# Optimization experiments

Measured on AMD Instinct MI355X. Metric: run time of the kernel, lower is better.

Reference implementation:

```python
import jax, jax.numpy as jnp
import numpy as np

N_HEADS = 8
HIDDEN = 256
D_HEAD = HIDDEN // N_HEADS
N_NODES = 4096
N_EDGES = 16384


def setup_inputs() -> dict:
    key = jax.random.key(0)
    ks = jax.random.split(key, 12)
    s = 0.05
    return {
        "q": jax.random.normal(ks[0], (N_EDGES, HIDDEN), jnp.float32),
        "k": jax.random.normal(ks[1], (N_NODES, HIDDEN), jnp.float32),
        "v": jax.random.normal(ks[2], (N_NODES, HIDDEN), jnp.float32),
        "T": jax.random.uniform(ks[3], (N_NODES, N_EDGES), jnp.float32),
        "Wq": jax.random.normal(ks[4], (HIDDEN, HIDDEN), jnp.float32) * s,
        "bq": jax.random.normal(ks[5], (HIDDEN,), jnp.float32) * s,
        "Wk": jax.random.normal(ks[6], (HIDDEN, HIDDEN), jnp.float32) * s,
        "bk": jax.random.normal(ks[7], (HIDDEN,), jnp.float32) * s,
        "Wv": jax.random.normal(ks[8], (HIDDEN, HIDDEN), jnp.float32) * s,
        "bv": jax.random.normal(ks[9], (HIDDEN,), jnp.float32) * s,
        "Wo": jax.random.normal(ks[10], (HIDDEN, HIDDEN), jnp.float32) * s,
        "bo": jax.random.normal(ks[11], (HIDDEN,), jnp.float32) * s,
    }


def reference(q, k, v, T, Wq, bq, Wk, bk, Wv, bv, Wo, bo):
    scale = D_HEAD ** (-0.5)
    # projections, reshaped to per-head layout
    qh = (q @ Wq.T + bq).reshape(-1, N_HEADS, D_HEAD)  # [E, H, d]
    kh = (k @ Wk.T + bk).reshape(-1, N_HEADS, D_HEAD)  # [N, H, d]
    vh = (v @ Wv.T + bv).reshape(-1, N_HEADS, D_HEAD)  # [N, H, d]
    # row-normalized transition matrix (rows with zero sum left unscaled)
    row_sum = jnp.sum(T, axis=-1, keepdims=True)       # [N, 1]
    Tn = T / jnp.where(row_sum == 0, 1.0, row_sum)     # [N, E]
    # edge->node aggregation of queries, then scale
    qn = jnp.einsum("ne,ehd->nhd", Tn, qh) * scale     # [N, H, d]
    # attention: full NxN scores per head
    scores = jnp.einsum("nhd,mhd->hnm", qn, kh)        # [H, N, N]
    attn = jax.nn.softmax(scores, axis=-1)
    ctx = jnp.einsum("hnm,mhd->nhd", attn, vh)         # [N, H, d]
    out = ctx.reshape(-1, N_HEADS * D_HEAD) @ Wo.T + bo  # [N, hidden]
    return out
```

## Files before the change

kernel.cpp:

```cpp
#include <hip/hip_runtime.h>


#define N_NODES 4096
#define N_EDGES 16384
#define HIDDEN  256
#define KSPLIT  16

typedef __attribute__((ext_vector_type(4))) float f32x4;
typedef __attribute__((ext_vector_type(8))) short s16x8;
typedef __attribute__((ext_vector_type(4))) unsigned short u16x4;
typedef __attribute__((ext_vector_type(8))) unsigned short u16x8;

__device__ __forceinline__ unsigned short f2bf(float f) {
    union { float f; unsigned u; } x; x.f = f;
    unsigned r = x.u + 0x7FFFu + ((x.u >> 16) & 1u);
    return (unsigned short)(r >> 16);
}
__device__ __forceinline__ s16x8 pack8s(f32x4 x, f32x4 y) {
    u16x8 o;
    o[0]=f2bf(x[0]); o[1]=f2bf(x[1]); o[2]=f2bf(x[2]); o[3]=f2bf(x[3]);
    o[4]=f2bf(y[0]); o[5]=f2bf(y[1]); o[6]=f2bf(y[2]); o[7]=f2bf(y[3]);
    union { u16x8 u; s16x8 s; } c; c.u = o; return c.s;
}

template<int MODE>
__global__ __launch_bounds__(256)
void proj_gemm(const float* __restrict__ A, const float* __restrict__ W,
               const float* __restrict__ bias, void* __restrict__ outp, int M)
{
    __shared__ __align__(16) float As[16][68];
    __shared__ __align__(16) float Ws[16][68];
    const int t  = threadIdx.x;
    const int bm = blockIdx.x * 64, bn = blockIdx.y * 64;
    const int tm = t & 15, tn = t >> 4;
    const int sm = t >> 2, skc = (t & 3) * 4;

    float c[4][4] = {};
    for (int k0 = 0; k0 < 256; k0 += 16) {
        f32x4 av = *(const f32x4*)&A[(long)(bm + sm) * 256 + k0 + skc];
        f32x4 wv = *(const f32x4*)&W[(bn + sm) * 256 + k0 + skc];
        __syncthreads();
        #pragma unroll
        for (int i = 0; i < 4; ++i) { As[skc + i][sm] = av[i]; Ws[skc + i][sm] = wv[i]; }
        __syncthreads();
        #pragma unroll
        for (int kk = 0; kk < 16; ++kk) {
            f32x4 a4 = *(const f32x4*)&As[kk][tm * 4];
            f32x4 w4 = *(const f32x4*)&Ws[kk][tn * 4];
            #pragma unroll
            for (int i = 0; i < 4; ++i)
                #pragma unroll
                for (int j = 0; j < 4; ++j)
                    c[i][j] = fmaf(a4[i], w4[j], c[i][j]);
        }
    }
    f32x4 b4 = *(const f32x4*)&bias[bn + tn * 4];
    if (MODE == 1) {
        unsigned short* out = (unsigned short*)outp;
        #pragma unroll
        for (int i = 0; i < 4; ++i) {
            u16x4 o;
            #pragma unroll
            for (int j = 0; j < 4; ++j) o[j] = f2bf(c[i][j] + b4[j]);
            *(u16x4*)&out[(long)(bm + tm * 4 + i) * 256 + bn + tn * 4] = o;
        }
    } else {
        unsigned short* out = (unsigned short*)outp;
        #pragma unroll
        for (int j = 0; j < 4; ++j) {
            u16x4 o;
            #pragma unroll
            for (int i = 0; i < 4; ++i) o[i] = f2bf(c[i][j] + b4[j]);
            *(u16x4*)&out[(long)(bn + tn * 4 + j) * M + bm + tm * 4] = o;
        }
    }
}

__global__ __launch_bounds__(256)
void proj_out_merge(const float* __restrict__ pctx, const float* __restrict__ plp,
                    const float* __restrict__ W, const float* __restrict__ bias,
                    float* __restrict__ out)
{
    __shared__ __align__(16) float As[16][68];
    __shared__ __align__(16) float Ws[16][68];
    const int t  = threadIdx.x;
    const int bm = blockIdx.x * 64, bn = blockIdx.y * 64;
    const int tm = t & 15, tn = t >> 4;
    const int sm = t >> 2, skc = (t & 3) * 4;
    const int row = bm + sm;

    float c[4][4] = {};
    for (int k0 = 0; k0 < 256; k0 += 16) {
        const int kk0 = k0 + skc, h = kk0 >> 5;
        f32x4 c0 = *(const f32x4*)&pctx[(long)row * 256 + kk0];
        f32x4 c1 = *(const f32x4*)&pctx[(long)(N_NODES + row) * 256 + kk0];
        float lsum = plp[h * N_NODES + row] + plp[(8 + h) * N_NODES + row];
        f32x4 av = (c0 + c1) * (1.0f / lsum);
        f32x4 wv = *(const f32x4*)&W[(bn + sm) * 256 + k0 + skc];
        __syncthreads();
        #pragma unroll
        for (int i = 0; i < 4; ++i) { As[skc + i][sm] = av[i]; Ws[skc + i][sm] = wv[i]; }
        __syncthreads();
        #pragma unroll
        for (int kk = 0; kk < 16; ++kk) {
            f32x4 a4 = *(const f32x4*)&As[kk][tm * 4];
            f32x4 w4 = *(const f32x4*)&Ws[kk][tn * 4];
            #pragma unroll
            for (int i = 0; i < 4; ++i)
                #pragma unroll
                for (int j = 0; j < 4; ++j)
                    c[i][j] = fmaf(a4[i], w4[j], c[i][j]);
        }
    }
    f32x4 b4 = *(const f32x4*)&bias[bn + tn * 4];
    #pragma unroll
    for (int i = 0; i < 4; ++i) {
        f32x4 o;
        #pragma unroll
        for (int j = 0; j < 4; ++j) o[j] = c[i][j] + b4[j];
        *(f32x4*)&out[(long)(bm + tm * 4 + i) * 256 + bn + tn * 4] = o;
    }
}

__global__ __launch_bounds__(512)
void proj_q_mfma(const float* __restrict__ A, const float* __restrict__ W,
                 const float* __restrict__ bias, unsigned short* __restrict__ outT)
{
    __shared__ __align__(16) unsigned short Wsm[256 * 264];
    __shared__ __align__(16) unsigned short Asm[64 * 72];
    const int t  = threadIdx.x;
    const int m0 = blockIdx.x * 64;

    const int am = t >> 3, akc = (t & 7) * 8;
    const float* Arow = &A[(long)(m0 + am) * 256];
    f32x4 a0 = *(const f32x4*)&Arow[akc];
    f32x4 a1 = *(const f32x4*)&Arow[akc + 4];

    #pragma unroll 4
    for (int i = 0; i < 32; ++i) {
        const int g = i * 512 + t;
        const int row = g >> 6, col = (g & 63) * 4;
        f32x4 w4 = *(const f32x4*)&W[row * 256 + col];
        u16x4 o;
        #pragma unroll
        for (int j = 0; j < 4; ++j) o[j] = f2bf(w4[j]);
        *(u16x4*)&Wsm[row * 264 + col] = o;
    }

    const int l = t & 63, lo = l & 15, h4 = l >> 4;
    const int wv = t >> 6, wm = (wv >> 2) * 32, wn = (wv & 3) * 64;
    f32x4 acc[2][4] = {};

    for (int k0 = 0; k0 < 4; ++k0) {
        u16x4 p0, p1;
        #pragma unroll
        for (int j = 0; j < 4; ++j) { p0[j] = f2bf(a0[j]); p1[j] = f2bf(a1[j]); }
        *(u16x4*)&Asm[am * 72 + akc]     = p0;
        *(u16x4*)&Asm[am * 72 + akc + 4] = p1;
        __syncthreads();
        if (k0 < 3) {
            a0 = *(const f32x4*)&Arow[(k0 + 1) * 64 + akc];
            a1 = *(const f32x4*)&Arow[(k0 + 1) * 64 + akc + 4];
        }
        s16x8 af[2][2], wf[4][2];
        #pragma unroll
        for (int mi = 0; mi < 2; ++mi)
            #pragma unroll
            for (int k2 = 0; k2 < 2; ++k2)
                af[mi][k2] = *(const s16x8*)&Asm[(wm + mi * 16 + lo) * 72 + k2 * 32 + h4 * 8];
        #pragma unroll
        for (int nj = 0; nj < 4; ++nj)
            #pragma unroll
            for (int k2 = 0; k2 < 2; ++k2)
                wf[nj][k2] = *(const s16x8*)&Wsm[(wn + nj * 16 + lo) * 264 + k0 * 64 + k2 * 32 + h4 * 8];
        #pragma unroll
        for (int k2 = 0; k2 < 2; ++k2)
            #pragma unroll
            for (int mi = 0; mi < 2; ++mi)
                #pragma unroll
                for (int nj = 0; nj < 4; ++nj)
                    acc[mi][nj] = __builtin_amdgcn_mfma_f32_16x16x32_bf16(
                        af[mi][k2], wf[nj][k2], acc[mi][nj], 0, 0, 0);
        __syncthreads();
    }
    float bi[4];
    #pragma unroll
    for (int nj = 0; nj < 4; ++nj) bi[nj] = bias[wn + nj * 16 + lo];
    #pragma unroll
    for (int mi = 0; mi < 2; ++mi)
        #pragma unroll
        for (int nj = 0; nj < 4; ++nj) {
            u16x4 o;
            #pragma unroll
            for (int r = 0; r < 4; ++r) o[r] = f2bf(acc[mi][nj][r] + bi[nj]);
            const int  n = wn + nj * 16 + lo;
            const long m = m0 + wm + mi * 16 + h4 * 4;
            *(u16x4*)&outT[(long)n * N_EDGES + m] = o;
        }
}

__global__ __launch_bounds__(512, 4)
void tgemm(const float* __restrict__ T, const unsigned short* __restrict__ Bt,
           float* __restrict__ part, float* __restrict__ rsp)
{
    __shared__ __align__(16) unsigned short Bsm[2][256 * 64];
    const int t  = threadIdx.x;
    const int ks = blockIdx.x & 15, ms = blockIdx.x >> 4;
    const int m0 = ms * 128;
    const long k00 = (long)ks * 1024;
    const int w = t >> 6, l = t & 63, lo = l & 15, h4 = l >> 4;

    const int kx = ((l & 7) * 8) ^ ((l >> 3) << 3);
    const unsigned short* Bsrc = Bt + k00 + kx;

#define STAGE(itv, bufv) do {                                                       \
    const unsigned short* _s = Bsrc + (long)(itv) * 64;                             \
    unsigned short* _d = &Bsm[(bufv)][w * 2048];                                    \
    _Pragma("unroll")                                                               \
    for (int _i = 0; _i < 4; ++_i)                                                  \
        __builtin_amdgcn_global_load_lds(                                           \
            (const __attribute__((address_space(1))) unsigned int*)                 \
                (_s + (long)(w * 32 + _i * 8 + (l >> 3)) * N_EDGES),                \
            (__attribute__((address_space(3))) unsigned int*)(_d + _i * 512),       \
            16, 0, 0);                                                              \
} while (0)

    const float* Arow = T + (long)(m0 + w * 16 + lo) * N_EDGES + k00 + h4 * 8;

    STAGE(0, 0);
    f32x4 a0 = *(const f32x4*)&Arow[0];
    f32x4 a1 = *(const f32x4*)&Arow[4];
    f32x4 a2 = *(const f32x4*)&Arow[32];
    f32x4 a3 = *(const f32x4*)&Arow[36];
    __syncthreads();

    f32x4 acc[16] = {};
    float rs = 0.f;

    for (int it = 0; it < 16; ++it) {
        const int cur = it & 1;
        if (it < 15) STAGE(it + 1, cur ^ 1);
        s16x8 af0 = pack8s(a0, a1);
        s16x8 af1 = pack8s(a2, a3);
        rs += a0[0]+a0[1]+a0[2]+a0[3] + a1[0]+a1[1]+a1[2]+a1[3]
            + a2[0]+a2[1]+a2[2]+a2[3] + a3[0]+a3[1]+a3[2]+a3[3];
        if (it < 15) {
            const float* An = Arow + (it + 1) * 64;
            a0 = *(const f32x4*)&An[0];
            a1 = *(const f32x4*)&An[4];
            a2 = *(const f32x4*)&An[32];
            a3 = *(const f32x4*)&An[36];
        }
        const unsigned short* Bb = Bsm[cur];
        const int swz = (lo & 7) << 3;
        #pragma unroll
        for (int nj = 0; nj < 16; ++nj) {
            const int jb = (nj * 16 + lo) * 64;
            s16x8 bf0 = *(const s16x8*)&Bb[jb + ((h4 * 8) ^ swz)];
            s16x8 bf1 = *(const s16x8*)&Bb[jb + ((32 + h4 * 8) ^ swz)];
            acc[nj] = __builtin_amdgcn_mfma_f32_16x16x32_bf16(af0, bf0, acc[nj], 0, 0, 0);
            acc[nj] = __builtin_amdgcn_mfma_f32_16x16x32_bf16(af1, bf1, acc[nj], 0, 0, 0);
        }
        __syncthreads();
    }
#undef STAGE

    rs += __shfl_xor(rs, 16); rs += __shfl_xor(rs, 32);
    if (h4 == 0) rsp[ks * N_NODES + m0 + w * 16 + lo] = rs;

    float* P = part + (long)ks * (N_NODES * HIDDEN);
    #pragma unroll
    for (int nj = 0; nj < 16; ++nj)
        #pragma unroll
        for (int r = 0; r < 4; ++r)
            P[(long)(m0 + w * 16 + h4 * 4 + r) * HIDDEN + nj * 16 + lo] = acc[nj][r];
}

__global__ __launch_bounds__(256)
void finalize(const float* __restrict__ part, const float* __restrict__ rsp,
              unsigned short* __restrict__ qn)
{
    const int idx = blockIdx.x * 256 + threadIdx.x;
    const long i4 = (long)idx * 4;
    const int n = (int)(i4 >> 8);
    f32x4 s = {};
    #pragma unroll
    for (int ksp = 0; ksp < KSPLIT; ++ksp)
        s += *(const f32x4*)&part[(long)ksp * (N_NODES * HIDDEN) + i4];
    float rs = 0.f;
    #pragma unroll
    for (int ksp = 0; ksp < KSPLIT; ++ksp) rs += rsp[ksp * N_NODES + n];
    rs = (rs == 0.0f) ? 1.0f : rs;
    const float sc = 0.17677669529663687f / rs;
    u16x4 o;
    #pragma unroll
    for (int i = 0; i < 4; ++i) o[i] = f2bf(s[i] * sc);
    *(u16x4*)&qn[i4] = o;
}

__global__ __launch_bounds__(256)
void attn(const unsigned short* __restrict__ qn, const unsigned short* __restrict__ kh,
          const unsigned short* __restrict__ vht, float* __restrict__ pctx,
          float* __restrict__ plp)
{
    __shared__ __align__(16) unsigned short Ksm[64 * 40];
    __shared__ __align__(16) unsigned short Vsm[32 * 72];
    __shared__ __align__(16) unsigned short Psm[4][32 * 72];
    const int t  = threadIdx.x;
    const int hh = blockIdx.x >> 6, nb = (blockIdx.x >> 1) & 31, mh = blockIdx.x & 1;
    const int w = t >> 6, l = t & 63, lo = l & 15, h4 = l >> 4;
    const int n0 = nb * 128 + w * 32;

    const int km = t >> 2, kdc = (t & 3) * 8;
    const int vd = t >> 3, vmc = (t & 7) * 8;

    s16x8 qf[2];
    #pragma unroll
    for (int ni = 0; ni < 2; ++ni)
        qf[ni] = *(const s16x8*)&qn[(long)(n0 + ni * 16 + lo) * HIDDEN + hh * 32 + h4 * 8];

    f32x4 acc[2][2] = {};
    float lp[2][4] = {};
    const f32x4 zero = {};

    for (int mt = mh * 32; mt < mh * 32 + 32; ++mt) {
        const int m0 = mt * 64;
        *(s16x8*)&Ksm[km * 40 + kdc] =
            *(const s16x8*)&kh[(long)(m0 + km) * HIDDEN + hh * 32 + kdc];
        *(s16x8*)&Vsm[vd * 72 + vmc] =
            *(const s16x8*)&vht[(long)(hh * 32 + vd) * N_NODES + m0 + vmc];
        __syncthreads();

        s16x8 kb[4];
        #pragma unroll
        for (int mi = 0; mi < 4; ++mi)
            kb[mi] = *(const s16x8*)&Ksm[(mi * 16 + lo) * 40 + h4 * 8];
        #pragma unroll
        for (int ni = 0; ni < 2; ++ni) {
            #pragma unroll
            for (int mi = 0; mi < 4; ++mi) {
                f32x4 s = __builtin_amdgcn_mfma_f32_16x16x32_bf16(qf[ni], kb[mi], zero, 0, 0, 0);
                #pragma unroll
                for (int r = 0; r < 4; ++r) {
                    float p = __expf(s[r]);
                    lp[ni][r] += p;
                    Psm[w][(ni * 16 + h4 * 4 + r) * 72 + mi * 16 + lo] = f2bf(p);
                }
            }
        }
        s16x8 pa[2][2], vb[2][2];
        #pragma unroll
        for (int ni = 0; ni < 2; ++ni)
            #pragma unroll
            for (int k2 = 0; k2 < 2; ++k2)
                pa[ni][k2] = *(const s16x8*)&Psm[w][(ni * 16 + lo) * 72 + k2 * 32 + h4 * 8];
        #pragma unroll
        for (int di = 0; di < 2; ++di)
            #pragma unroll
            for (int k2 = 0; k2 < 2; ++k2)
                vb[di][k2] = *(const s16x8*)&Vsm[(di * 16 + lo) * 72 + k2 * 32 + h4 * 8];
        #pragma unroll
        for (int k2 = 0; k2 < 2; ++k2)
            #pragma unroll
            for (int ni = 0; ni < 2; ++ni)
                #pragma unroll
                for (int di = 0; di < 2; ++di)
                    acc[ni][di] = __builtin_amdgcn_mfma_f32_16x16x32_bf16(
                        pa[ni][k2], vb[di][k2], acc[ni][di], 0, 0, 0);
        __syncthreads();
    }
    #pragma unroll
    for (int ni = 0; ni < 2; ++ni)
        #pragma unroll
        for (int r = 0; r < 4; ++r) {
            float v2 = lp[ni][r];
            v2 += __shfl_xor(v2, 1); v2 += __shfl_xor(v2, 2);
            v2 += __shfl_xor(v2, 4); v2 += __shfl_xor(v2, 8);
            lp[ni][r] = v2;
        }
    float* myctx = pctx + (long)mh * (N_NODES * HIDDEN);
    float* myplp = plp  + (long)(mh * 8 + hh) * N_NODES;
    if (lo == 0)
        #pragma unroll
        for (int ni = 0; ni < 2; ++ni)
            #pragma unroll
            for (int r = 0; r < 4; ++r)
                myplp[n0 + ni * 16 + h4 * 4 + r] = lp[ni][r];
    #pragma unroll
    for (int ni = 0; ni < 2; ++ni)
        #pragma unroll
        for (int di = 0; di < 2; ++di)
            #pragma unroll
            for (int r = 0; r < 4; ++r)
                myctx[(long)(n0 + ni * 16 + h4 * 4 + r) * HIDDEN + hh * 32 + di * 16 + lo]
                    = acc[ni][di][r];
}

extern "C" void kernel_launch(void* const* d_in, const int* in_sizes, int n_in,
                              void* d_out, int out_size, void* d_ws, size_t ws_size,
                              hipStream_t stream)
{
    const float* q  = (const float*)d_in[0];
    const float* k  = (const float*)d_in[1];
    const float* v  = (const float*)d_in[2];
    const float* T  = (const float*)d_in[3];
    const float* Wq = (const float*)d_in[4];  const float* bq = (const float*)d_in[5];
    const float* Wk = (const float*)d_in[6];  const float* bk = (const float*)d_in[7];
    const float* Wv = (const float*)d_in[8];  const float* bv = (const float*)d_in[9];
    const float* Wo = (const float*)d_in[10]; const float* bo = (const float*)d_in[11];

    char* w = (char*)d_ws;
    unsigned short* qh_t = (unsigned short*)(w);
    unsigned short* kh   = (unsigned short*)(w + (8u  << 20));
    unsigned short* vh_t = (unsigned short*)(w + (10u << 20));
    unsigned short* qn   = (unsigned short*)(w + (12u << 20));
    float*          pctx = (float*)         (w + (14u << 20));
    float*          plp  = (float*)         (w + (22u << 20));
    float*          part = (float*)         (w + (24u << 20));
    float*          rsp  = (float*)         (w + (88u << 20));

    proj_q_mfma<<<256, 512, 0, stream>>>(q, Wq, bq, qh_t);
    proj_gemm<1><<<dim3(64, 4),  256, 0, stream>>>(k, Wk, bk, kh,   N_NODES);
    proj_gemm<2><<<dim3(64, 4),  256, 0, stream>>>(v, Wv, bv, vh_t, N_NODES);
    tgemm<<<512, 512, 0, stream>>>(T, qh_t, part, rsp);
    finalize<<<1024, 256, 0, stream>>>(part, rsp, qn);
    attn<<<512, 256, 0, stream>>>(qn, kh, vh_t, pctx, plp);
    proj_out_merge<<<dim3(64, 4), 256, 0, stream>>>(pctx, plp, Wo, bo, (float*)d_out);
}
```

Measured before the change: 230.8 us.

## Move projections to bf16 MFMA and split attention keys four ways

Adds a kernel that converts all four weight matrices to bf16 once, then replaces the fp32 FMA GEMMs for the K, V and output projections, and the LDS-staged Q projection, with register-only MFMA kernels that read A directly from global memory. The attention grid doubles to 1024 blocks, each covering a quarter of the key range, and the output projection now merges four partial contexts and softmax denominators. The aim is to raise matrix-core use and occupancy in the projections and attention. In exchange it adds a kernel launch, more partial-sum memory traffic, and fp32 inputs rounded to bf16 in the K, V and output projections.

```diff
diff --git a/kernel.cpp b/kernel.cpp
--- a/kernel.cpp
+++ b/kernel.cpp
@@ -23,180 +23,105 @@
     union { u16x8 u; s16x8 s; } c; c.u = o; return c.s;
 }
 
+__global__ __launch_bounds__(256)
+void cvtW(const float* __restrict__ Wq, const float* __restrict__ Wk,
+          const float* __restrict__ Wv, const float* __restrict__ Wo,
+          unsigned short* __restrict__ dst)
+{
+    const int g = blockIdx.x * 256 + threadIdx.x;
+    const long base = (long)g * 8;
+    const int mat = (int)(base >> 16), off = (int)(base & 65535);
+    const float* src = (mat == 0) ? Wq : (mat == 1) ? Wk : (mat == 2) ? Wv : Wo;
+    f32x4 x = *(const f32x4*)&src[off];
+    f32x4 y = *(const f32x4*)&src[off + 4];
+    union { u16x8 u; s16x8 s; } c; c.s = pack8s(x, y);
+    *(u16x8*)&dst[base] = c.u;
+}
+
 template<int MODE>
 __global__ __launch_bounds__(256)
-void proj_gemm(const float* __restrict__ A, const float* __restrict__ W,
-               const float* __restrict__ bias, void* __restrict__ outp, int M)
-{
-    __shared__ __align__(16) float As[16][68];
-    __shared__ __align__(16) float Ws[16][68];
-    const int t  = threadIdx.x;
-    const int bm = blockIdx.x * 64, bn = blockIdx.y * 64;
-    const int tm = t & 15, tn = t >> 4;
-    const int sm = t >> 2, skc = (t & 3) * 4;
-
-    float c[4][4] = {};
-    for (int k0 = 0; k0 < 256; k0 += 16) {
-        f32x4 av = *(const f32x4*)&A[(long)(bm + sm) * 256 + k0 + skc];
-        f32x4 wv = *(const f32x4*)&W[(bn + sm) * 256 + k0 + skc];
-        __syncthreads();
-        #pragma unroll
-        for (int i = 0; i < 4; ++i) { As[skc + i][sm] = av[i]; Ws[skc + i][sm] = wv[i]; }
-        __syncthreads();
-        #pragma unroll
-        for (int kk = 0; kk < 16; ++kk) {
-            f32x4 a4 = *(const f32x4*)&As[kk][tm * 4];
-            f32x4 w4 = *(const f32x4*)&Ws[kk][tn * 4];
-            #pragma unroll
-            for (int i = 0; i < 4; ++i)
-                #pragma unroll
-                for (int j = 0; j < 4; ++j)
-                    c[i][j] = fmaf(a4[i], w4[j], c[i][j]);
-        }
-    }
-    f32x4 b4 = *(const f32x4*)&bias[bn + tn * 4];
-    if (MODE == 1) {
-        unsigned short* out = (unsigned short*)outp;
-        #pragma unroll
-        for (int i = 0; i < 4; ++i) {
+void proj_mfma(const float* __restrict__ A, const unsigned short* __restrict__ Wbf,
+               const float* __restrict__ bias, unsigned short* __restrict__ out, int M)
+{
+    const int t = threadIdx.x;
+    const int w = t >> 6, l = t & 63, lo = l & 15, h4 = l >> 4;
+    const int m0 = blockIdx.x * 64 + w * 16;
+    const int bn = blockIdx.y * 64;
+    const float* Ar = A + (long)(m0 + lo) * 256 + h4 * 8;
+
+    f32x4 acc[4] = {};
+    #pragma unroll
+    for (int kk = 0; kk < 8; ++kk) {
+        f32x4 x = *(const f32x4*)&Ar[kk * 32];
+        f32x4 y = *(const f32x4*)&Ar[kk * 32 + 4];
+        s16x8 af = pack8s(x, y);
+        #pragma unroll
+        for (int nj = 0; nj < 4; ++nj) {
+            s16x8 bf = *(const s16x8*)&Wbf[(bn + nj * 16 + lo) * 256 + kk * 32 + h4 * 8];
+            acc[nj] = __builtin_amdgcn_mfma_f32_16x16x32_bf16(af, bf, acc[nj], 0, 0, 0);
+        }
+    }
+    #pragma unroll
+    for (int nj = 0; nj < 4; ++nj) {
+        const int n = bn + nj * 16 + lo;
+        const float bi = bias[n];
+        if (MODE == 1) {
+            #pragma unroll
+            for (int r = 0; r < 4; ++r)
+                out[(long)(m0 + h4 * 4 + r) * 256 + n] = f2bf(acc[nj][r] + bi);
+        } else {
             u16x4 o;
             #pragma unroll
-            for (int j = 0; j < 4; ++j) o[j] = f2bf(c[i][j] + b4[j]);
-            *(u16x4*)&out[(long)(bm + tm * 4 + i) * 256 + bn + tn * 4] = o;
-        }
-    } else {
-        unsigned short* out = (unsigned short*)outp;
-        #pragma unroll
-        for (int j = 0; j < 4; ++j) {
-            u16x4 o;
-            #pragma unroll
-            for (int i = 0; i < 4; ++i) o[i] = f2bf(c[i][j] + b4[j]);
-            *(u16x4*)&out[(long)(bn + tn * 4 + j) * M + bm + tm * 4] = o;
-        }
-    }
-}
-
-__global__ __launch_bounds__(256)
-void proj_out_merge(const float* __restrict__ pctx, const float* __restrict__ plp,
-                    const float* __restrict__ W, const float* __restrict__ bias,
-                    float* __restrict__ out)
-{
-    __shared__ __align__(16) float As[16][68];
-    __shared__ __align__(16) float Ws[16][68];
-    const int t  = threadIdx.x;
-    const int bm = blockIdx.x * 64, bn = blockIdx.y * 64;
-    const int tm = t & 15, tn = t >> 4;
-    const int sm = t >> 2, skc = (t & 3) * 4;
-    const int row = bm + sm;
-
-    float c[4][4] = {};
-    for (int k0 = 0; k0 < 256; k0 += 16) {
-        const int kk0 = k0 + skc, h = kk0 >> 5;
-        f32x4 c0 = *(const f32x4*)&pctx[(long)row * 256 + kk0];
-        f32x4 c1 = *(const f32x4*)&pctx[(long)(N_NODES + row) * 256 + kk0];
-        float lsum = plp[h * N_NODES + row] + plp[(8 + h) * N_NODES + row];
-        f32x4 av = (c0 + c1) * (1.0f / lsum);
-        f32x4 wv = *(const f32x4*)&W[(bn + sm) * 256 + k0 + skc];
-        __syncthreads();
-        #pragma unroll
-        for (int i = 0; i < 4; ++i) { As[skc + i][sm] = av[i]; Ws[skc + i][sm] = wv[i]; }
-        __syncthreads();
-        #pragma unroll
-        for (int kk = 0; kk < 16; ++kk) {
-            f32x4 a4 = *(const f32x4*)&As[kk][tm * 4];
-            f32x4 w4 = *(const f32x4*)&Ws[kk][tn * 4];
-            #pragma unroll
-            for (int i = 0; i < 4; ++i)
-                #pragma unroll
-                for (int j = 0; j < 4; ++j)
-                    c[i][j] = fmaf(a4[i], w4[j], c[i][j]);
-        }
-    }
-    f32x4 b4 = *(const f32x4*)&bias[bn + tn * 4];
-    #pragma unroll
-    for (int i = 0; i < 4; ++i) {
-        f32x4 o;
-        #pragma unroll
-        for (int j = 0; j < 4; ++j) o[j] = c[i][j] + b4[j];
-        *(f32x4*)&out[(long)(bm + tm * 4 + i) * 256 + bn + tn * 4] = o;
-    }
-}
-
-__global__ __launch_bounds__(512)
-void proj_q_mfma(const float* __restrict__ A, const float* __restrict__ W,
-                 const float* __restrict__ bias, unsigned short* __restrict__ outT)
-{
-    __shared__ __align__(16) unsigned short Wsm[256 * 264];
-    __shared__ __align__(16) unsigned short Asm[64 * 72];
-    const int t  = threadIdx.x;
-    const int m0 = blockIdx.x * 64;
-
-    const int am = t >> 3, akc = (t & 7) * 8;
-    const float* Arow = &A[(long)(m0 + am) * 256];
-    f32x4 a0 = *(const f32x4*)&Arow[akc];
-    f32x4 a1 = *(const f32x4*)&Arow[akc + 4];
-
-    #pragma unroll 4
-    for (int i = 0; i < 32; ++i) {
-        const int g = i * 512 + t;
-        const int row = g >> 6, col = (g & 63) * 4;
-        f32x4 w4 = *(const f32x4*)&W[row * 256 + col];
-        u16x4 o;
-        #pragma unroll
-        for (int j = 0; j < 4; ++j) o[j] = f2bf(w4[j]);
-        *(u16x4*)&Wsm[row * 264 + col] = o;
-    }
-
-    const int l = t & 63, lo = l & 15, h4 = l >> 4;
-    const int wv = t >> 6, wm = (wv >> 2) * 32, wn = (wv & 3) * 64;
-    f32x4 acc[2][4] = {};
-
-    for (int k0 = 0; k0 < 4; ++k0) {
-        u16x4 p0, p1;
-        #pragma unroll
-        for (int j = 0; j < 4; ++j) { p0[j] = f2bf(a0[j]); p1[j] = f2bf(a1[j]); }
-        *(u16x4*)&Asm[am * 72 + akc]     = p0;
-        *(u16x4*)&Asm[am * 72 + akc + 4] = p1;
-        __syncthreads();
-        if (k0 < 3) {
-            a0 = *(const f32x4*)&Arow[(k0 + 1) * 64 + akc];
-            a1 = *(const f32x4*)&Arow[(k0 + 1) * 64 + akc + 4];
-        }
-        s16x8 af[2][2], wf[4][2];
-        #pragma unroll
-        for (int mi = 0; mi < 2; ++mi)
-            #pragma unroll
-            for (int k2 = 0; k2 < 2; ++k2)
-                af[mi][k2] = *(const s16x8*)&Asm[(wm + mi * 16 + lo) * 72 + k2 * 32 + h4 * 8];
-        #pragma unroll
-        for (int nj = 0; nj < 4; ++nj)
-            #pragma unroll
-            for (int k2 = 0; k2 < 2; ++k2)
-                wf[nj][k2] = *(const s16x8*)&Wsm[(wn + nj * 16 + lo) * 264 + k0 * 64 + k2 * 32 + h4 * 8];
-        #pragma unroll
-        for (int k2 = 0; k2 < 2; ++k2)
-            #pragma unroll
-            for (int mi = 0; mi < 2; ++mi)
-                #pragma unroll
-                for (int nj = 0; nj < 4; ++nj)
-                    acc[mi][nj] = __builtin_amdgcn_mfma_f32_16x16x32_bf16(
-                        af[mi][k2], wf[nj][k2], acc[mi][nj], 0, 0, 0);
-        __syncthreads();
-    }
-    float bi[4];
-    #pragma unroll
-    for (int nj = 0; nj < 4; ++nj) bi[nj] = bias[wn + nj * 16 + lo];
-    #pragma unroll
-    for (int mi = 0; mi < 2; ++mi)
+            for (int r = 0; r < 4; ++r) o[r] = f2bf(acc[nj][r] + bi);
+            *(u16x4*)&out[(long)n * M + m0 + h4 * 4] = o;
+        }
+    }
+}
+
+__global__ __launch_bounds__(256)
+void proj_out_mfma(const float* __restrict__ pctx, const float* __restrict__ plp,
+                   const unsigned short* __restrict__ Wobf, const float* __restrict__ bo,
+                   float* __restrict__ out)
+{
+    const int t = threadIdx.x;
+    const int w = t >> 6, l = t & 63, lo = l & 15, h4 = l >> 4;
+    const int m0 = blockIdx.x * 64 + w * 16;
+    const int bn = blockIdx.y * 64;
+    const int m = m0 + lo;
+
+    float inv[8];
+    #pragma unroll
+    for (int h = 0; h < 8; ++h) {
+        float s = plp[(0 * 8 + h) * N_NODES + m] + plp[(1 * 8 + h) * N_NODES + m]
+                + plp[(2 * 8 + h) * N_NODES + m] + plp[(3 * 8 + h) * N_NODES + m];
+        inv[h] = 1.0f / s;
+    }
+    const float* P = pctx + (long)m * 256;
+    const long PS = (long)N_NODES * 256;
+
+    f32x4 acc[4] = {};
+    #pragma unroll
+    for (int kk = 0; kk < 8; ++kk) {
+        const int off = kk * 32 + h4 * 8;
+        f32x4 x = *(const f32x4*)&P[off]          + *(const f32x4*)&P[PS + off]
+                + *(const f32x4*)&P[2 * PS + off] + *(const f32x4*)&P[3 * PS + off];
+        f32x4 y = *(const f32x4*)&P[off + 4]          + *(const f32x4*)&P[PS + off + 4]
+                + *(const f32x4*)&P[2 * PS + off + 4] + *(const f32x4*)&P[3 * PS + off + 4];
+        s16x8 af = pack8s(x * inv[kk], y * inv[kk]);
         #pragma unroll
         for (int nj = 0; nj < 4; ++nj) {
-            u16x4 o;
-            #pragma unroll
-            for (int r = 0; r < 4; ++r) o[r] = f2bf(acc[mi][nj][r] + bi[nj]);
-            const int  n = wn + nj * 16 + lo;
-            const long m = m0 + wm + mi * 16 + h4 * 4;
-            *(u16x4*)&outT[(long)n * N_EDGES + m] = o;
-        }
+            s16x8 bf = *(const s16x8*)&Wobf[(bn + nj * 16 + lo) * 256 + kk * 32 + h4 * 8];
+            acc[nj] = __builtin_amdgcn_mfma_f32_16x16x32_bf16(af, bf, acc[nj], 0, 0, 0);
+        }
+    }
+    #pragma unroll
+    for (int nj = 0; nj < 4; ++nj) {
+        const int n = bn + nj * 16 + lo;
+        const float bi = bo[n];
+        #pragma unroll
+        for (int r = 0; r < 4; ++r)
+            out[(long)(m0 + h4 * 4 + r) * 256 + n] = acc[nj][r] + bi;
+    }
 }
 
 __global__ __launch_bounds__(512, 4)
@@ -307,7 +232,7 @@
     __shared__ __align__(16) unsigned short Vsm[32 * 72];
     __shared__ __align__(16) unsigned short Psm[4][32 * 72];
     const int t  = threadIdx.x;
-    const int hh = blockIdx.x >> 6, nb = (blockIdx.x >> 1) & 31, mh = blockIdx.x & 1;
+    const int hh = blockIdx.x >> 7, nb = (blockIdx.x >> 2) & 31, mh = blockIdx.x & 3;
     const int w = t >> 6, l = t & 63, lo = l & 15, h4 = l >> 4;
     const int n0 = nb * 128 + w * 32;
 
@@ -323,7 +248,7 @@
     float lp[2][4] = {};
     const f32x4 zero = {};
 
-    for (int mt = mh * 32; mt < mh * 32 + 32; ++mt) {
+    for (int mt = mh * 16; mt < mh * 16 + 16; ++mt) {
         const int m0 = mt * 64;
         *(s16x8*)&Ksm[km * 40 + kdc] =
             *(const s16x8*)&kh[(long)(m0 + km) * HIDDEN + hh * 32 + kdc];
@@ -415,15 +340,21 @@
     unsigned short* vh_t = (unsigned short*)(w + (10u << 20));
     unsigned short* qn   = (unsigned short*)(w + (12u << 20));
     float*          pctx = (float*)         (w + (14u << 20));
-    float*          plp  = (float*)         (w + (22u << 20));
-    float*          part = (float*)         (w + (24u << 20));
-    float*          rsp  = (float*)         (w + (88u << 20));
-
-    proj_q_mfma<<<256, 512, 0, stream>>>(q, Wq, bq, qh_t);
-    proj_gemm<1><<<dim3(64, 4),  256, 0, stream>>>(k, Wk, bk, kh,   N_NODES);
-    proj_gemm<2><<<dim3(64, 4),  256, 0, stream>>>(v, Wv, bv, vh_t, N_NODES);
+    float*          plp  = (float*)         (w + (30u << 20));
+    float*          part = (float*)         (w + (32u << 20));
+    float*          rsp  = (float*)         (w + (96u << 20));
+    unsigned short* wbf  = (unsigned short*)(w + (97u << 20));
+    unsigned short* wq_bf = wbf;
+    unsigned short* wk_bf = wbf + 65536;
+    unsigned short* wv_bf = wbf + 2 * 65536;
+    unsigned short* wo_bf = wbf + 3 * 65536;
+
+    cvtW<<<128, 256, 0, stream>>>(Wq, Wk, Wv, Wo, wbf);
+    proj_mfma<2><<<dim3(256, 4), 256, 0, stream>>>(q, wq_bf, bq, qh_t, N_EDGES);
+    proj_mfma<1><<<dim3(64, 4),  256, 0, stream>>>(k, wk_bf, bk, kh,   N_NODES);
+    proj_mfma<2><<<dim3(64, 4),  256, 0, stream>>>(v, wv_bf, bv, vh_t, N_NODES);
     tgemm<<<512, 512, 0, stream>>>(T, qh_t, part, rsp);
     finalize<<<1024, 256, 0, stream>>>(part, rsp, qn);
-    attn<<<512, 256, 0, stream>>>(qn, kh, vh_t, pctx, plp);
-    proj_out_merge<<<dim3(64, 4), 256, 0, stream>>>(pctx, plp, Wo, bo, (float*)d_out);
-}
+    attn<<<1024, 256, 0, stream>>>(qn, kh, vh_t, pctx, plp);
+    proj_out_mfma<<<dim3(64, 4), 256, 0, stream>>>(pctx, plp, wo_bf, bo, (float*)d_out);
+}
```

Measured after the change: 214.7 us. 1.07x faster.
